# Kernel optimization log

Hardware: AMD Instinct MI355X
Metric: run time of the kernel (lower is better)

## Reference

```python
import jax, jax.numpy as jnp
import numpy as np

NH = 16
NKV = 4
ROPE_BASE = 10000.0
ROPE_TSL = 1024
EPS = 1.1920928955078125e-07  # torch fp32 finfo eps (F.rms_norm default)


def _rms_norm(t):
    return t * jax.lax.rsqrt(jnp.mean(t * t, axis=-1, keepdims=True) + EPS)


def _rope_tables(T, hd):
    # Rotary with rd = hd (rope_dims=0 -> full-head rope). NTK rescale if T > tsl.
    rd = hd
    if T > ROPE_TSL:
        base = ROPE_BASE * (T / ROPE_TSL) ** (rd / (rd - 2))
    else:
        base = ROPE_BASE
    inv_freq = 1.0 / base ** (np.arange(0, rd, 2, dtype=np.float32) / rd)
    t = np.arange(T, dtype=np.float32)
    fr = np.outer(t, inv_freq)  # [T, hd//2]
    return jnp.asarray(np.cos(fr)), jnp.asarray(np.sin(fr))


def _apply_rope(x, cos, sin):
    # x: [B,T,H,D]; cos/sin: [T, D//2] broadcast over batch & heads
    h = x.shape[-1] // 2
    x1, x2 = x[..., :h], x[..., h:]
    c = cos[None, :, None, :]
    s = sin[None, :, None, :]
    return jnp.concatenate((x1 * c + x2 * s, -x1 * s + x2 * c), axis=-1)


def setup_inputs() -> dict:
    key = jax.random.key(0)
    k1, k2, k3, k4, k5 = jax.random.split(key, 5)
    B, T, dim = 2, 2048, 2048
    hd = dim // NH
    kd = NKV * hd
    std = 0.02
    return {
        "x": jax.random.normal(k1, (B, T, dim), dtype=jnp.float32),
        "Wq": jax.random.normal(k2, (dim, dim), dtype=jnp.float32) * std,
        "Wk": jax.random.normal(k3, (kd, dim), dtype=jnp.float32) * std,
        "Wv": jax.random.normal(k4, (kd, dim), dtype=jnp.float32) * std,
        "Wp": jax.random.normal(k5, (dim, dim), dtype=jnp.float32) * std,
        "q_gain": jnp.full((NH,), 1.5, dtype=jnp.float32),
    }


def reference(x, Wq, Wk, Wv, Wp, q_gain):
    B, T, d = x.shape
    hd = d // NH
    g = NH // NKV
    q = (x @ Wq.T).reshape(B, T, NH, hd)
    k = (x @ Wk.T).reshape(B, T, NKV, hd)
    v = (x @ Wv.T).reshape(B, T, NKV, hd)
    q = _rms_norm(q)
    k = _rms_norm(k)
    cos, sin = _rope_tables(T, hd)
    q = _apply_rope(q, cos, sin)
    k = _apply_rope(k, cos, sin)
    q = q * q_gain[None, None, :, None]
    # GQA causal SDPA: group queries per kv head
    qg = q.reshape(B, T, NKV, g, hd)
    scores = jnp.einsum("btkgd,bskd->bkgts", qg, k) / jnp.sqrt(jnp.asarray(hd, x.dtype))
    causal = jnp.tril(jnp.ones((T, T), dtype=bool))
    scores = jnp.where(causal[None, None, None, :, :], scores, jnp.asarray(-jnp.inf, scores.dtype))
    attn = jax.nn.softmax(scores, axis=-1)
    y = jnp.einsum("bkgts,bskd->btkgd", attn, v).reshape(B, T, d)
    return y @ Wp.T
```

## Files before the change

kernel.cpp:

```cpp
#include <hip/hip_runtime.h>
#include <math.h>

#define NH 16
#define NKV 4
#define HD 128
#define DIM 2048
#define GQ 4
#define EPS 1.1920928955078125e-07f

typedef unsigned short u16;
using bf16x8 = __attribute__((ext_vector_type(8))) short;
using f16x4  = __attribute__((ext_vector_type(4))) _Float16;
using f32x4  = __attribute__((ext_vector_type(4))) float;

__device__ inline float fast_exp2(float x) { return __builtin_amdgcn_exp2f(x); }

__device__ inline short f2bf(float f) {
    unsigned u = __builtin_bit_cast(unsigned, f);
    return (short)((u + 0x7FFFu + ((u >> 16) & 1u)) >> 16);
}
__device__ inline u16 f2h(float f) {
    _Float16 h = (_Float16)f;
    return __builtin_bit_cast(u16, h);
}

#define ASYNC_LOAD16(g, l)                                                        \
    __builtin_amdgcn_global_load_lds(                                             \
        (const __attribute__((address_space(1))) unsigned*)(g),                   \
        (__attribute__((address_space(3))) unsigned*)(l), 16, 0, 0)

#define SCHED_FENCE() __builtin_amdgcn_sched_barrier(0)
#define WAIT_LGKM0()  asm volatile("s_waitcnt lgkmcnt(0)" ::: "memory")
#define WAIT_VM(N)    asm volatile("s_waitcnt vmcnt(" #N ")" ::: "memory")

__global__ __launch_bounds__(256) void cvt_fused(
    const float* __restrict__ x,  const float* __restrict__ wq,
    const float* __restrict__ wk, const float* __restrict__ wv,
    const float* __restrict__ wp,
    u16* __restrict__ x16, u16* __restrict__ wqkv, u16* __restrict__ wp16,
    int nx4, int total) {
    int i = blockIdx.x * 256 + threadIdx.x;
    if (i >= total) return;
    const int nw4 = DIM * DIM / 4;
    const int nk4 = (NKV * HD) * DIM / 4;
    const float4* s4;
    ushort4* d4;
    if (i < nx4) {
        s4 = (const float4*)x + i; d4 = (ushort4*)x16 + i;
    } else {
        int j = i - nx4;
        if (j < nw4) {
            s4 = (const float4*)wq + j; d4 = (ushort4*)wqkv + j;
        } else {
            j -= nw4;
            if (j < nk4) {
                s4 = (const float4*)wk + j;
                d4 = (ushort4*)wqkv + (size_t)2048 * DIM / 4 + j;
            } else {
                j -= nk4;
                if (j < nk4) {
                    s4 = (const float4*)wv + j;
                    d4 = (ushort4*)wqkv + (size_t)2560 * DIM / 4 + j;
                } else {
                    j -= nk4;
                    s4 = (const float4*)wp + j; d4 = (ushort4*)wp16 + j;
                }
            }
        }
    }
    float4 f = *s4;
    ushort4 o;
    o.x = (u16)f2bf(f.x); o.y = (u16)f2bf(f.y);
    o.z = (u16)f2bf(f.z); o.w = (u16)f2bf(f.w);
    *d4 = o;
}

__global__ __launch_bounds__(256) void rope_tab(float* __restrict__ ct,
                                                float* __restrict__ st,
                                                float l2b64) {
    const int idx = blockIdx.x * 256 + threadIdx.x;
    const int t = idx >> 6;
    const int j = idx & 63;
    const float inv_freq = fast_exp2(-(float)j * l2b64);
    const float fr = (float)t * inv_freq;
    ct[idx] = cosf(fr);
    st[idx] = sinf(fr);
}

#define BN 256
#define BKT 64
#define NKT (DIM / BKT)

template <int EPI, int MT>
__global__ __launch_bounds__(512, 2) void gemm256(
    const u16* __restrict__ A, const u16* __restrict__ W,
    float* __restrict__ C, int N,
    u16* __restrict__ q16, u16* __restrict__ k16,
    u16* __restrict__ vt16,
    const float* __restrict__ ctab, const float* __restrict__ stab,
    const float* __restrict__ q_gain, int T) {
    __shared__ u16 As[2][MT * 64 * BKT];
    __shared__ u16 Bs[2][BN * BKT];

    const int tid  = threadIdx.x;
    const int wid  = tid >> 6;
    const int lane = tid & 63;
    const int l16  = lane & 15;
    const int quad = lane >> 4;
    const int wm   = wid >> 1;
    const int wn   = wid & 1;
    const int m0   = blockIdx.x * (MT * 64);
    const int n0   = blockIdx.y * BN;
    const int K    = DIM;

    const int srow = lane >> 3;
    const int scol = ((lane & 7) ^ srow) * 8;
    const u16* pa = A + (size_t)(m0 + srow) * K + scol;
    const u16* pw = W + (size_t)(n0 + srow) * K + scol;

    const int ca0 = ((quad)     ^ (l16 & 7)) * 8;
    const int ca1 = ((4 + quad) ^ (l16 & 7)) * 8;

    f32x4 acc[MT][8];
#pragma unroll
    for (int i = 0; i < MT; i++)
#pragma unroll
        for (int j = 0; j < 8; j++) acc[i][j] = (f32x4){0.f, 0.f, 0.f, 0.f};

#pragma unroll
    for (int r = 0; r < MT; r++)
        ASYNC_LOAD16(pa + (size_t)(r * 64 + wid * 8) * K, &As[0][(r * 64 + wid * 8) * BKT]);
    ASYNC_LOAD16(pw + (size_t)(0 * 64 + wid * 8) * K, &Bs[0][(0 * 64 + wid * 8) * BKT]);
    ASYNC_LOAD16(pw + (size_t)(2 * 64 + wid * 8) * K, &Bs[0][(2 * 64 + wid * 8) * BKT]);
    ASYNC_LOAD16(pw + (size_t)(1 * 64 + wid * 8) * K, &Bs[0][(1 * 64 + wid * 8) * BKT]);
    ASYNC_LOAD16(pw + (size_t)(3 * 64 + wid * 8) * K, &Bs[0][(3 * 64 + wid * 8) * BKT]);
    WAIT_VM(2);
    SCHED_FENCE();
    __builtin_amdgcn_s_barrier();
    SCHED_FENCE();

#pragma unroll 1
    for (int kt = 0; kt < NKT; kt++) {
        const int cur = kt & 1;
        const u16* Ac = &As[cur][0];
        const u16* Bc = &Bs[cur][0];
        u16* An = &As[cur ^ 1][0];
        u16* Bn = &Bs[cur ^ 1][0];
        const size_t ko = (size_t)((kt + 1) & (NKT - 1)) * BKT;

        bf16x8 a0[MT], a1[MT];

        {
            bf16x8 bf[4];
#pragma unroll
            for (int mt = 0; mt < MT; mt++)
                a0[mt] = *(const bf16x8*)&Ac[(wm * (MT * 16) + mt * 16 + l16) * BKT + ca0];
#pragma unroll
            for (int nt = 0; nt < 4; nt++)
                bf[nt] = *(const bf16x8*)&Bc[(wn * 128 + nt * 16 + l16) * BKT + ca0];
#pragma unroll
            for (int r = 0; r < MT; r++)
                ASYNC_LOAD16(pa + (size_t)(r * 64 + wid * 8) * K + ko,
                             &An[(r * 64 + wid * 8) * BKT]);
            SCHED_FENCE();
            __builtin_amdgcn_s_barrier();
            WAIT_LGKM0();
            SCHED_FENCE();
            __builtin_amdgcn_s_setprio(1);
#pragma unroll
            for (int mt = 0; mt < MT; mt++)
#pragma unroll
                for (int nt = 0; nt < 4; nt++)
                    acc[mt][nt] = __builtin_amdgcn_mfma_f32_16x16x32_bf16(
                        a0[mt], bf[nt], acc[mt][nt], 0, 0, 0);
            __builtin_amdgcn_s_setprio(0);
            SCHED_FENCE();
            __builtin_amdgcn_s_barrier();
        }

        {
            bf16x8 bf[4];
#pragma unroll
            for (int mt = 0; mt < MT; mt++)
                a1[mt] = *(const bf16x8*)&Ac[(wm * (MT * 16) + mt * 16 + l16) * BKT + ca1];
#pragma unroll
            for (int nt = 0; nt < 4; nt++)
                bf[nt] = *(const bf16x8*)&Bc[(wn * 128 + nt * 16 + l16) * BKT + ca1];
            ASYNC_LOAD16(pw + (size_t)(0 * 64 + wid * 8) * K + ko,
                         &Bn[(0 * 64 + wid * 8) * BKT]);
            ASYNC_LOAD16(pw + (size_t)(2 * 64 + wid * 8) * K + ko,
                         &Bn[(2 * 64 + wid * 8) * BKT]);
            SCHED_FENCE();
            __builtin_amdgcn_s_barrier();
            WAIT_LGKM0();
            SCHED_FENCE();
            __builtin_amdgcn_s_setprio(1);
#pragma unroll
            for (int mt = 0; mt < MT; mt++)
#pragma unroll
                for (int nt = 0; nt < 4; nt++)
                    acc[mt][nt] = __builtin_amdgcn_mfma_f32_16x16x32_bf16(
                        a1[mt], bf[nt], acc[mt][nt], 0, 0, 0);
            __builtin_amdgcn_s_setprio(0);
            if constexpr (MT == 4) { WAIT_VM(6); } else { WAIT_VM(4); }
            SCHED_FENCE();
            __builtin_amdgcn_s_barrier();
            SCHED_FENCE();
        }

        {
            bf16x8 bf[4];
#pragma unroll
            for (int nt = 0; nt < 4; nt++)
                bf[nt] = *(const bf16x8*)&Bc[(wn * 128 + (nt + 4) * 16 + l16) * BKT + ca0];
            ASYNC_LOAD16(pw + (size_t)(1 * 64 + wid * 8) * K + ko,
                         &Bn[(1 * 64 + wid * 8) * BKT]);
            ASYNC_LOAD16(pw + (size_t)(3 * 64 + wid * 8) * K + ko,
                         &Bn[(3 * 64 + wid * 8) * BKT]);
            SCHED_FENCE();
            __builtin_amdgcn_s_barrier();
            WAIT_LGKM0();
            SCHED_FENCE();
            __builtin_amdgcn_s_setprio(1);
#pragma unroll
            for (int mt = 0; mt < MT; mt++)
#pragma unroll
                for (int nt = 0; nt < 4; nt++)
                    acc[mt][nt + 4] = __builtin_amdgcn_mfma_f32_16x16x32_bf16(
                        a0[mt], bf[nt], acc[mt][nt + 4], 0, 0, 0);
            __builtin_amdgcn_s_setprio(0);
            SCHED_FENCE();
            __builtin_amdgcn_s_barrier();
        }

        {
            bf16x8 bf[4];
#pragma unroll
            for (int nt = 0; nt < 4; nt++)
                bf[nt] = *(const bf16x8*)&Bc[(wn * 128 + (nt + 4) * 16 + l16) * BKT + ca1];
            SCHED_FENCE();
            __builtin_amdgcn_s_barrier();
            WAIT_LGKM0();
            SCHED_FENCE();
            __builtin_amdgcn_s_setprio(1);
#pragma unroll
            for (int mt = 0; mt < MT; mt++)
#pragma unroll
                for (int nt = 0; nt < 4; nt++)
                    acc[mt][nt + 4] = __builtin_amdgcn_mfma_f32_16x16x32_bf16(
                        a1[mt], bf[nt], acc[mt][nt + 4], 0, 0, 0);
            __builtin_amdgcn_s_setprio(0);
            WAIT_VM(2);
            SCHED_FENCE();
            __builtin_amdgcn_s_barrier();
            SCHED_FENCE();
        }
    }
    WAIT_VM(0);

    if constexpr (EPI == 0) {
#pragma unroll
        for (int mt = 0; mt < MT; mt++)
#pragma unroll
            for (int nt = 0; nt < 8; nt++)
#pragma unroll
                for (int r = 0; r < 4; r++)
                    C[(size_t)(m0 + wm * (MT * 16) + mt * 16 + quad * 4 + r) * N +
                      n0 + wn * 128 + nt * 16 + l16] = acc[mt][nt][r];
    } else {
        const int nb = n0 + wn * 128;
        if (nb < 2560) {
            const bool isQ = (nb < 2048);
            const float gval =
                isQ ? (q_gain[nb >> 7] * 0.08838834764831843f * 1.4426950408889634f)
                    : 1.0f;
#pragma unroll
            for (int mt = 0; mt < MT; mt++) {
#pragma unroll
                for (int r = 0; r < 4; r++) {
                    float s = 0.f;
#pragma unroll
                    for (int nt = 0; nt < 8; nt++) {
                        float a = acc[mt][nt][r];
                        s = fmaf(a, a, s);
                    }
                    s += __shfl_xor(s, 1);
                    s += __shfl_xor(s, 2);
                    s += __shfl_xor(s, 4);
                    s += __shfl_xor(s, 8);
                    const float scale = rsqrtf(s * (1.0f / HD) + EPS) * gval;
                    const int m = m0 + wm * (MT * 16) + mt * 16 + quad * 4 + r;
                    const int t = m & (T - 1);
                    const float* ct = ctab + t * 64;
                    const float* st = stab + t * 64;
                    u16* dst = isQ ? (q16 + (size_t)m * 2048 + nb)
                                   : (k16 + (size_t)m * 512 + (nb - 2048));
#pragma unroll
                    for (int nt = 0; nt < 4; nt++) {
                        const int j = nt * 16 + l16;
                        const float c = ct[j], sn = st[j];
                        const float x1 = acc[mt][nt][r] * scale;
                        const float x2 = acc[mt][nt + 4][r] * scale;
                        dst[j]      = (u16)f2bf(x1 * c + x2 * sn);
                        dst[j + 64] = (u16)f2bf(x2 * c - x1 * sn);
                    }
                }
            }
        } else {
#pragma unroll
            for (int mt = 0; mt < MT; mt++) {
                const int mb = m0 + wm * (MT * 16) + mt * 16 + quad * 4;
                const int b = mb >> 11;
                const int t0 = mb & (T - 1);
#pragma unroll
                for (int nt = 0; nt < 8; nt++) {
                    const int dcol = nb - 2560 + nt * 16 + l16;
                    const int kvh = dcol >> 7;
                    const int d = dcol & (HD - 1);
                    ushort4 o;
                    o.x = f2h(acc[mt][nt][0]);
                    o.y = f2h(acc[mt][nt][1]);
                    o.z = f2h(acc[mt][nt][2]);
                    o.w = f2h(acc[mt][nt][3]);
                    *(ushort4*)(vt16 + ((size_t)((b * NKV + kvh) * HD + d)) * T + t0) = o;
                }
            }
        }
    }
}

#define QT 128
#define SK 64

__global__ __launch_bounds__(512) void flash5(const u16* __restrict__ q16,
                                              const u16* __restrict__ k16,
                                              const u16* __restrict__ vt16,
                                              u16* __restrict__ y16, int T) {
    __shared__ u16 Ks[2][SK * 128];
    __shared__ u16 Vt[2][HD * 64];

    const int tid = threadIdx.x;
    const int wave = tid >> 6;
    const int lane = tid & 63;
    const int l16 = lane & 15;
    const int quad = lane >> 4;

    const int bid = blockIdx.x;
    const int bh = bid & 31;
    const int qi = bid >> 5;
    const int nqt = T / QT;
    const int qt = (qi < (nqt >> 1)) ? qi : (nqt - 1 - (qi - (nqt >> 1)));
    const int h = bh & 15;
    const int b = bh >> 4;
    const int kv = h / GQ;

    const u16* kg = k16 + ((size_t)b * T * NKV + kv) * HD;
    const u16* vg = vt16 + (size_t)(b * NKV + kv) * HD * T;

    const int krow_in_seg = lane >> 4;
    const int kclog_base = lane & 15;
    const int vrow_in_seg = lane >> 3;
    const int vclog = (lane & 7) ^ (lane >> 3);

    const int q0 = qt * QT;
    const int qglob = q0 + wave * 16 + l16;
    const int nts = q0 / SK + 2;

    bf16x8 qf[4];
    {
        const u16* qp = q16 + ((size_t)(b * T + qglob) * NH + h) * HD;
#pragma unroll
        for (int kc = 0; kc < 4; kc++)
            qf[kc] = *(const bf16x8*)(qp + kc * 32 + quad * 8);
    }

    f32x4 of[8];
#pragma unroll
    for (int i = 0; i < 8; i++) of[i] = (f32x4){0.f, 0.f, 0.f, 0.f};
    float m_i = -1e30f, l_i = 0.0f;

#pragma unroll
    for (int j = 0; j < 2; j++) {
        const int seg = wave * 2 + j;
        const int r = seg * 4 + krow_in_seg;
        const int clog = kclog_base ^ (r & 15);
        ASYNC_LOAD16(kg + (size_t)r * (NKV * HD) + clog * 8, &Ks[0][seg * 512]);
        const int d = seg * 8 + vrow_in_seg;
        ASYNC_LOAD16(vg + (size_t)d * T + vclog * 8, &Vt[0][seg * 512]);
    }

    for (int it = 0; it < nts; it++) {
        const int cur = it & 1;
        __syncthreads();

        if (it + 1 < nts) {
            const int s1 = (it + 1) * SK;
#pragma unroll
            for (int j = 0; j < 2; j++) {
                const int seg = wave * 2 + j;
                const int r = seg * 4 + krow_in_seg;
                const int clog = kclog_base ^ (r & 15);
                ASYNC_LOAD16(kg + (size_t)(s1 + r) * (NKV * HD) + clog * 8,
                             &Ks[cur ^ 1][seg * 512]);
                const int d = seg * 8 + vrow_in_seg;
                ASYNC_LOAD16(vg + (size_t)d * T + s1 + vclog * 8,
                             &Vt[cur ^ 1][seg * 512]);
            }
        }

        if (it == nts - 1 && wave < 4) continue;

        f32x4 sf[4];
#pragma unroll
        for (int st = 0; st < 4; st++) sf[st] = (f32x4){0.f, 0.f, 0.f, 0.f};
#pragma unroll
        for (int kc = 0; kc < 4; kc++)
#pragma unroll
            for (int st = 0; st < 4; st++) {
                const int row = st * 16 + l16;
                bf16x8 kf = *(const bf16x8*)
                    &Ks[cur][row * 128 + (((kc * 4 + quad) ^ l16) * 8)];
                sf[st] = __builtin_amdgcn_mfma_f32_16x16x32_bf16(kf, qf[kc], sf[st], 0, 0, 0);
            }

        if (it >= nts - 2) {
            const int s0 = it * SK;
#pragma unroll
            for (int st = 0; st < 4; st++)
#pragma unroll
                for (int r = 0; r < 4; r++)
                    if (s0 + st * 16 + quad * 4 + r > qglob) sf[st][r] = -1e30f;
        }

        float tm = -1e30f;
#pragma unroll
        for (int st = 0; st < 4; st++)
#pragma unroll
            for (int r = 0; r < 4; r++) tm = fmaxf(tm, sf[st][r]);
        tm = fmaxf(tm, __shfl_xor(tm, 16));
        tm = fmaxf(tm, __shfl_xor(tm, 32));

        if (__ballot(tm > m_i + 8.0f)) {
            const float mnew = fmaxf(m_i, tm);
            const float alpha = fast_exp2(m_i - mnew);
            m_i = mnew;
            l_i *= alpha;
#pragma unroll
            for (int dt = 0; dt < 8; dt++)
#pragma unroll
                for (int r = 0; r < 4; r++) of[dt][r] *= alpha;
        }

        f16x4 pf[4];
        float ls = 0.0f;
#pragma unroll
        for (int st = 0; st < 4; st++)
#pragma unroll
            for (int r = 0; r < 4; r++) {
                float e = fast_exp2(sf[st][r] - m_i);
                ls += e;
                pf[st][r] = (_Float16)e;
            }
        ls += __shfl_xor(ls, 16);
        ls += __shfl_xor(ls, 32);
        l_i += ls;

#pragma unroll
        for (int st = 0; st < 4; st++) {
            const int clog = st * 2 + (quad >> 1);
#pragma unroll
            for (int dt = 0; dt < 8; dt++) {
                const int d = dt * 16 + l16;
                const int phys = clog ^ (l16 & 7);
                f16x4 va = *(const f16x4*)
                    &Vt[cur][d * 64 + phys * 8 + (quad & 1) * 4];
                of[dt] = __builtin_amdgcn_mfma_f32_16x16x16f16(va, pf[st], of[dt], 0, 0, 0);
            }
        }
    }

    const float inv = 1.0f / l_i;
    u16* yp = y16 + ((size_t)(b * T + qglob) * NH + h) * HD + quad * 4;
#pragma unroll
    for (int dt = 0; dt < 8; dt++) {
        ushort4 o;
        o.x = (u16)f2bf(of[dt][0] * inv);
        o.y = (u16)f2bf(of[dt][1] * inv);
        o.z = (u16)f2bf(of[dt][2] * inv);
        o.w = (u16)f2bf(of[dt][3] * inv);
        *(ushort4*)(yp + dt * 16) = o;
    }
}

extern "C" void kernel_launch(void* const* d_in, const int* in_sizes, int n_in,
                              void* d_out, int out_size, void* d_ws, size_t ws_size,
                              hipStream_t stream) {
    const float* x      = (const float*)d_in[0];
    const float* Wq     = (const float*)d_in[1];
    const float* Wk     = (const float*)d_in[2];
    const float* Wv     = (const float*)d_in[3];
    const float* Wp     = (const float*)d_in[4];
    const float* q_gain = (const float*)d_in[5];
    float* out = (float*)d_out;

    const int B = 2;
    const int BT = in_sizes[0] / DIM;
    const int T = BT / B;
    const int KD = NKV * HD;

    u16* x16   = (u16*)d_ws;
    u16* wqkv  = x16 + (size_t)BT * DIM;
    u16* wp16  = wqkv + (size_t)3072 * DIM;
    u16* q16   = wp16 + (size_t)DIM * DIM;
    u16* k16   = q16 + (size_t)BT * DIM;
    u16* vt16  = k16 + (size_t)BT * KD;
    float* ctab = (float*)(vt16 + (size_t)BT * KD);
    float* stab = ctab + (size_t)T * 64;
    u16* y16   = x16;

    double base = 10000.0;
    if (T > 1024) base = 10000.0 * pow((double)T / 1024.0, 128.0 / 126.0);
    const float l2b64 = (float)(log2(base) / 64.0);

    const int nx4  = BT * DIM / 4;
    const int total4 = nx4 + 2 * (DIM * DIM / 4) + 2 * (KD * DIM / 4);

    cvt_fused<<<(total4 + 255) / 256, 256, 0, stream>>>(
        x, Wq, Wk, Wv, Wp, x16, wqkv, wp16, nx4, total4);
    rope_tab<<<(T * 64 + 255) / 256, 256, 0, stream>>>(ctab, stab, l2b64);

    gemm256<1, 4><<<dim3(BT / 256, 3072 / BN), 512, 0, stream>>>(
        x16, wqkv, nullptr, 0, q16, k16, vt16, ctab, stab, q_gain, T);

    flash5<<<32 * (T / QT), 512, 0, stream>>>(q16, k16, vt16, y16, T);

    gemm256<0, 2><<<dim3(BT / 128, DIM / BN), 512, 0, stream>>>(
        y16, wp16, out, DIM, nullptr, nullptr, nullptr, nullptr, nullptr, nullptr, T);
}
```

Before: 304.0 us.

## Software-pipeline flash attention QK and PV across tiles; fuse rope table into convert

Restructures the attention loop so each iteration computes the QK scores for the next tile while finishing softmax and PV for the previous tile. It uses a triple-buffered V tile and s_setprio around the MFMA blocks so matrix work can overlap the exp/softmax arithmetic. It also folds the rope table generation into the fp32-to-bf16 conversion launch, which removes one kernel launch. The costs are more registers (two score sets live at once, with launch_bounds asking for 4 blocks) and more LDS for the third V buffer, which may reduce occupancy.

```diff
diff --git a/kernel.cpp b/kernel.cpp
--- a/kernel.cpp
+++ b/kernel.cpp
@@ -38,7 +38,18 @@
     const float* __restrict__ wk, const float* __restrict__ wv,
     const float* __restrict__ wp,
     u16* __restrict__ x16, u16* __restrict__ wqkv, u16* __restrict__ wp16,
-    int nx4, int total) {
+    float* __restrict__ ct, float* __restrict__ st, float l2b64,
+    int nx4, int total, int nblk_cvt) {
+    if ((int)blockIdx.x >= nblk_cvt) {
+        const int idx = (blockIdx.x - nblk_cvt) * 256 + threadIdx.x;
+        const int t = idx >> 6;
+        const int j = idx & 63;
+        const float inv_freq = fast_exp2(-(float)j * l2b64);
+        const float fr = (float)t * inv_freq;
+        ct[idx] = cosf(fr);
+        st[idx] = sinf(fr);
+        return;
+    }
     int i = blockIdx.x * 256 + threadIdx.x;
     if (i >= total) return;
     const int nw4 = DIM * DIM / 4;
@@ -75,18 +86,6 @@
     *d4 = o;
 }
 
-__global__ __launch_bounds__(256) void rope_tab(float* __restrict__ ct,
-                                                float* __restrict__ st,
-                                                float l2b64) {
-    const int idx = blockIdx.x * 256 + threadIdx.x;
-    const int t = idx >> 6;
-    const int j = idx & 63;
-    const float inv_freq = fast_exp2(-(float)j * l2b64);
-    const float fr = (float)t * inv_freq;
-    ct[idx] = cosf(fr);
-    st[idx] = sinf(fr);
-}
-
 #define BN 256
 #define BKT 64
 #define NKT (DIM / BKT)
@@ -332,12 +331,12 @@
 #define QT 128
 #define SK 64
 
-__global__ __launch_bounds__(512) void flash5(const u16* __restrict__ q16,
-                                              const u16* __restrict__ k16,
-                                              const u16* __restrict__ vt16,
-                                              u16* __restrict__ y16, int T) {
+__global__ __launch_bounds__(512, 4) void flash6(const u16* __restrict__ q16,
+                                                 const u16* __restrict__ k16,
+                                                 const u16* __restrict__ vt16,
+                                                 u16* __restrict__ y16, int T) {
     __shared__ u16 Ks[2][SK * 128];
-    __shared__ u16 Vt[2][HD * 64];
+    __shared__ u16 Vt[3][HD * 64];
 
     const int tid = threadIdx.x;
     const int wave = tid >> 6;
@@ -389,94 +388,117 @@
         ASYNC_LOAD16(vg + (size_t)d * T + vclog * 8, &Vt[0][seg * 512]);
     }
 
-    for (int it = 0; it < nts; it++) {
-        const int cur = it & 1;
+    auto finishTile = [&](f32x4 (&SF)[4], int vbuf) {
+        float tm = fmaxf(fmaxf(SF[0][0], SF[0][1]), SF[0][2]);
+        tm = fmaxf(fmaxf(tm, SF[0][3]), SF[1][0]);
+        tm = fmaxf(fmaxf(tm, SF[1][1]), SF[1][2]);
+        tm = fmaxf(fmaxf(tm, SF[1][3]), SF[2][0]);
+        tm = fmaxf(fmaxf(tm, SF[2][1]), SF[2][2]);
+        tm = fmaxf(fmaxf(tm, SF[2][3]), SF[3][0]);
+        tm = fmaxf(fmaxf(tm, SF[3][1]), SF[3][2]);
+        tm = fmaxf(tm, SF[3][3]);
+        tm = fmaxf(tm, __shfl_xor(tm, 16));
+        tm = fmaxf(tm, __shfl_xor(tm, 32));
+
+        if (__ballot(tm > m_i + 8.0f)) {
+            const float mnew = fmaxf(m_i, tm);
+            const float alpha = fast_exp2(m_i - mnew);
+            m_i = mnew;
+            l_i *= alpha;
+#pragma unroll
+            for (int dt = 0; dt < 8; dt++)
+#pragma unroll
+                for (int r = 0; r < 4; r++) of[dt][r] *= alpha;
+        }
+
+        f16x4 pf[4];
+        float ls = 0.0f;
+#pragma unroll
+        for (int st = 0; st < 4; st++)
+#pragma unroll
+            for (int r = 0; r < 4; r++) {
+                float e = fast_exp2(SF[st][r] - m_i);
+                ls += e;
+                pf[st][r] = (_Float16)e;
+            }
+        ls += __shfl_xor(ls, 16);
+        ls += __shfl_xor(ls, 32);
+        l_i += ls;
+
+        const u16* Vb = &Vt[vbuf][0];
+        __builtin_amdgcn_s_setprio(1);
+#pragma unroll
+        for (int st = 0; st < 4; st++) {
+            const int clog = st * 2 + (quad >> 1);
+#pragma unroll
+            for (int dt = 0; dt < 8; dt++) {
+                const int d = dt * 16 + l16;
+                const int phys = clog ^ (l16 & 7);
+                f16x4 va = *(const f16x4*)
+                    &Vb[d * 64 + phys * 8 + (quad & 1) * 4];
+                of[dt] = __builtin_amdgcn_mfma_f32_16x16x16f16(va, pf[st], of[dt], 0, 0, 0);
+            }
+        }
+        __builtin_amdgcn_s_setprio(0);
+    };
+
+    auto body = [&](int it, f32x4 (&SFN)[4], f32x4 (&SFP)[4]) {
+        const int kcur = it & 1;
         __syncthreads();
 
         if (it + 1 < nts) {
             const int s1 = (it + 1) * SK;
+            const int kn = (it + 1) & 1;
+            const int vn = (it + 1) % 3;
 #pragma unroll
             for (int j = 0; j < 2; j++) {
                 const int seg = wave * 2 + j;
                 const int r = seg * 4 + krow_in_seg;
                 const int clog = kclog_base ^ (r & 15);
                 ASYNC_LOAD16(kg + (size_t)(s1 + r) * (NKV * HD) + clog * 8,
-                             &Ks[cur ^ 1][seg * 512]);
+                             &Ks[kn][seg * 512]);
                 const int d = seg * 8 + vrow_in_seg;
                 ASYNC_LOAD16(vg + (size_t)d * T + s1 + vclog * 8,
-                             &Vt[cur ^ 1][seg * 512]);
-            }
-        }
-
-        if (it == nts - 1 && wave < 4) continue;
-
-        f32x4 sf[4];
-#pragma unroll
-        for (int st = 0; st < 4; st++) sf[st] = (f32x4){0.f, 0.f, 0.f, 0.f};
-#pragma unroll
-        for (int kc = 0; kc < 4; kc++)
-#pragma unroll
-            for (int st = 0; st < 4; st++) {
-                const int row = st * 16 + l16;
-                bf16x8 kf = *(const bf16x8*)
-                    &Ks[cur][row * 128 + (((kc * 4 + quad) ^ l16) * 8)];
-                sf[st] = __builtin_amdgcn_mfma_f32_16x16x32_bf16(kf, qf[kc], sf[st], 0, 0, 0);
-            }
-
-        if (it >= nts - 2) {
-            const int s0 = it * SK;
-#pragma unroll
-            for (int st = 0; st < 4; st++)
-#pragma unroll
-                for (int r = 0; r < 4; r++)
-                    if (s0 + st * 16 + quad * 4 + r > qglob) sf[st][r] = -1e30f;
-        }
-
-        float tm = -1e30f;
-#pragma unroll
-        for (int st = 0; st < 4; st++)
-#pragma unroll
-            for (int r = 0; r < 4; r++) tm = fmaxf(tm, sf[st][r]);
-        tm = fmaxf(tm, __shfl_xor(tm, 16));
-        tm = fmaxf(tm, __shfl_xor(tm, 32));
-
-        if (__ballot(tm > m_i + 8.0f)) {
-            const float mnew = fmaxf(m_i, tm);
-            const float alpha = fast_exp2(m_i - mnew);
-            m_i = mnew;
-            l_i *= alpha;
-#pragma unroll
-            for (int dt = 0; dt < 8; dt++)
-#pragma unroll
-                for (int r = 0; r < 4; r++) of[dt][r] *= alpha;
-        }
-
-        f16x4 pf[4];
-        float ls = 0.0f;
-#pragma unroll
-        for (int st = 0; st < 4; st++)
-#pragma unroll
-            for (int r = 0; r < 4; r++) {
-                float e = fast_exp2(sf[st][r] - m_i);
-                ls += e;
-                pf[st][r] = (_Float16)e;
-            }
-        ls += __shfl_xor(ls, 16);
-        ls += __shfl_xor(ls, 32);
-        l_i += ls;
-
-#pragma unroll
-        for (int st = 0; st < 4; st++) {
-            const int clog = st * 2 + (quad >> 1);
-#pragma unroll
-            for (int dt = 0; dt < 8; dt++) {
-                const int d = dt * 16 + l16;
-                const int phys = clog ^ (l16 & 7);
-                f16x4 va = *(const f16x4*)
-                    &Vt[cur][d * 64 + phys * 8 + (quad & 1) * 4];
-                of[dt] = __builtin_amdgcn_mfma_f32_16x16x16f16(va, pf[st], of[dt], 0, 0, 0);
-            }
-        }
+                             &Vt[vn][seg * 512]);
+            }
+        }
+
+        if (!(it == nts - 1 && wave < 4)) {
+#pragma unroll
+            for (int st = 0; st < 4; st++) SFN[st] = (f32x4){0.f, 0.f, 0.f, 0.f};
+            __builtin_amdgcn_s_setprio(1);
+#pragma unroll
+            for (int kc = 0; kc < 4; kc++)
+#pragma unroll
+                for (int st = 0; st < 4; st++) {
+                    const int row = st * 16 + l16;
+                    bf16x8 kf = *(const bf16x8*)
+                        &Ks[kcur][row * 128 + (((kc * 4 + quad) ^ l16) * 8)];
+                    SFN[st] = __builtin_amdgcn_mfma_f32_16x16x32_bf16(kf, qf[kc], SFN[st], 0, 0, 0);
+                }
+            __builtin_amdgcn_s_setprio(0);
+            if (it >= nts - 2) {
+                const int s0 = it * SK;
+#pragma unroll
+                for (int st = 0; st < 4; st++)
+#pragma unroll
+                    for (int r = 0; r < 4; r++)
+                        if (s0 + st * 16 + quad * 4 + r > qglob) SFN[st][r] = -1e30f;
+            }
+        }
+
+        if (it > 0) finishTile(SFP, (it - 1) % 3);
+    };
+
+    f32x4 sfA[4], sfB[4];
+#pragma unroll 1
+    for (int i2 = 0; i2 < nts; i2 += 2) {
+        body(i2, sfA, sfB);
+        if (i2 + 1 < nts) body(i2 + 1, sfB, sfA);
+    }
+    if (wave >= 4) {
+        if (nts & 1) finishTile(sfA, (nts - 1) % 3);
+        else         finishTile(sfB, (nts - 1) % 3);
     }
 
     const float inv = 1.0f / l_i;
@@ -524,15 +546,16 @@
 
     const int nx4  = BT * DIM / 4;
     const int total4 = nx4 + 2 * (DIM * DIM / 4) + 2 * (KD * DIM / 4);
-
-    cvt_fused<<<(total4 + 255) / 256, 256, 0, stream>>>(
-        x, Wq, Wk, Wv, Wp, x16, wqkv, wp16, nx4, total4);
-    rope_tab<<<(T * 64 + 255) / 256, 256, 0, stream>>>(ctab, stab, l2b64);
+    const int nblk_cvt = (total4 + 255) / 256;
+    const int nblk_rope = (T * 64 + 255) / 256;
+
+    cvt_fused<<<nblk_cvt + nblk_rope, 256, 0, stream>>>(
+        x, Wq, Wk, Wv, Wp, x16, wqkv, wp16, ctab, stab, l2b64, nx4, total4, nblk_cvt);
 
     gemm256<1, 4><<<dim3(BT / 256, 3072 / BN), 512, 0, stream>>>(
         x16, wqkv, nullptr, 0, q16, k16, vt16, ctab, stab, q_gain, T);
 
-    flash5<<<32 * (T / QT), 512, 0, stream>>>(q16, k16, vt16, y16, T);
+    flash6<<<32 * (T / QT), 512, 0, stream>>>(q16, k16, vt16, y16, T);
 
     gemm256<0, 2><<<dim3(BT / 128, DIM / BN), 512, 0, stream>>>(
         y16, wp16, out, DIM, nullptr, nullptr, nullptr, nullptr, nullptr, nullptr, T);
```

Result: slower. 328.1 us (+7.9%).
